# Optimization experiments

Measured on AMD Instinct MI355X. Metric: run time of the kernel, lower is better.

## Reference

```python
import jax, jax.numpy as jnp
import numpy as np

VOCAB = 32000
EMB = 1024
BLOCK = 2048
B = 4


def setup_inputs() -> dict:
    key = jax.random.key(0)
    ks = jax.random.split(key, 10)
    s = EMB ** -0.5
    return {
        "idx": jax.random.randint(ks[0], (B, BLOCK), 0, VOCAB),
        "targets": jax.random.randint(ks[1], (B, BLOCK), 0, VOCAB),
        "tok_emb": jax.random.normal(ks[2], (VOCAB, EMB), jnp.float32),
        "pos_emb": jax.random.normal(ks[3], (BLOCK, EMB), jnp.float32),
        "Wk": jax.random.normal(ks[4], (EMB, EMB), jnp.float32) * s,
        "Wq": jax.random.normal(ks[5], (EMB, EMB), jnp.float32) * s,
        "Wv": jax.random.normal(ks[6], (EMB, EMB), jnp.float32) * s,
        "Wlm": jax.random.normal(ks[7], (EMB, VOCAB), jnp.float32) * s,
        "blm": jnp.zeros((VOCAB,), jnp.float32),
    }


def reference(idx, targets, tok_emb, pos_emb, Wk, Wq, Wv, Wlm, blm):
    B_, T = idx.shape
    x = tok_emb[idx] + pos_emb[:T]  # [B,T,C]
    C = x.shape[-1]
    k = x @ Wk  # [B,T,H]
    q = x @ Wq
    v = x @ Wv
    wei = jnp.einsum("bth,bsh->bts", q, k) * (C ** -0.5)  # [B,T,T]
    causal = jnp.tril(jnp.ones((T, T), bool))
    wei = jnp.where(causal, wei, -jnp.inf)
    wei = jax.nn.softmax(wei, axis=-1)
    out = jnp.einsum("bts,bsh->bth", wei, v)  # [B,T,H]
    logits = out @ Wlm + blm  # [B,T,V]
    logits2d = logits.reshape(B_ * T, -1)
    tgt = targets.reshape(B_ * T)
    logp = jax.nn.log_softmax(logits2d, axis=-1)
    loss = -jnp.mean(jnp.take_along_axis(logp, tgt[:, None], axis=1))
    return logits2d, loss
```

## Files before the change

kernel.cpp:

```cpp
#include <hip/hip_runtime.h>
#include <hip/hip_bf16.h>
#include <cstdint>

#define VOCAB 32000
#define EMB   1024
#define TLEN  2048
#define NB    4
#define MTOT  (NB*TLEN)

typedef __bf16 bf16;
typedef __bf16 bf16x8 __attribute__((ext_vector_type(8)));
typedef float  f32x4  __attribute__((ext_vector_type(4)));

__global__ void embed_kernel(const int* __restrict__ idx,
                             const float* __restrict__ tok,
                             const float* __restrict__ pos,
                             bf16* __restrict__ x)
{
    int gid = blockIdx.x * 256 + threadIdx.x;
    int r   = gid >> 7;
    int c0  = (gid & 127) << 3;
    int t   = r & (TLEN - 1);
    int tk  = idx[r];
    const float4* tp = reinterpret_cast<const float4*>(tok + (long)tk * EMB + c0);
    const float4* pp = reinterpret_cast<const float4*>(pos + (long)t  * EMB + c0);
    float4 a0 = tp[0], a1 = tp[1];
    float4 b0 = pp[0], b1 = pp[1];
    bf16x8 o;
    o[0] = (bf16)(a0.x + b0.x); o[1] = (bf16)(a0.y + b0.y);
    o[2] = (bf16)(a0.z + b0.z); o[3] = (bf16)(a0.w + b0.w);
    o[4] = (bf16)(a1.x + b1.x); o[5] = (bf16)(a1.y + b1.y);
    o[6] = (bf16)(a1.z + b1.z); o[7] = (bf16)(a1.w + b1.w);
    *reinterpret_cast<bf16x8*>(x + (long)r * EMB + c0) = o;
}

__global__ void transpose_conv_kernel(const float* __restrict__ W,
                                      bf16* __restrict__ Wt,
                                      int Kdim, int Ndim)
{
    __shared__ bf16 tile[64][65];
    int n0 = blockIdx.x * 64;
    int k0 = blockIdx.y * 64;
    int tid = threadIdx.x;
    int c  = tid & 63, r0 = tid >> 6;
#pragma unroll
    for (int i = 0; i < 16; ++i) {
        int r = r0 + i * 4;
        tile[r][c] = (bf16)W[(long)(k0 + r) * Ndim + n0 + c];
    }
    __syncthreads();
    int kc = tid & 63, nr0 = tid >> 6;
#pragma unroll
    for (int i = 0; i < 16; ++i) {
        int nr = nr0 + i * 4;
        Wt[(long)(n0 + nr) * Kdim + k0 + kc] = tile[kc][nr];
    }
}

__device__ __forceinline__ void gll16(const void* g, void* l)
{
    __builtin_amdgcn_global_load_lds(
        (const __attribute__((address_space(1))) unsigned int*)g,
        (__attribute__((address_space(3))) unsigned int*)l, 16, 0, 0);
}

template<int OMODE>
__global__ __launch_bounds__(256)
void gemm_bt_kernel(const bf16* __restrict__ A, int lda, long sA,
                    const bf16* __restrict__ Bt, int ldb, long sB,
                    void* __restrict__ Cv, int ldc, long sC,
                    int K, const float* __restrict__ bias)
{
    __shared__ bf16 As[128 * 32];
    __shared__ bf16 Bs[128 * 32];

    const int tid  = threadIdx.x;
    const int lane = tid & 63;
    const int wv   = tid >> 6;
    const int wr   = wv >> 1, wc = wv & 1;
    const long zb  = blockIdx.z;

    const bf16* Ab = A  + zb * sA + (long)(blockIdx.y * 128) * lda;
    const bf16* Bb = Bt + zb * sB + (long)(blockIdx.x * 128) * ldb;

    f32x4 acc[4][4] = {};

    const int l0 = tid, l1 = tid + 256;
    const int r0s = l0 >> 2, kg0 = (l0 & 3) * 8;
    const int r1s = l1 >> 2, kg1 = (l1 & 3) * 8;

    for (int kt = 0; kt < K; kt += 32) {
        if (kt) __syncthreads();
        gll16(Ab + (long)r0s * lda + kt + kg0, &As[l0 * 8]);
        gll16(Ab + (long)r1s * lda + kt + kg1, &As[l1 * 8]);
        gll16(Bb + (long)r0s * ldb + kt + kg0, &Bs[l0 * 8]);
        gll16(Bb + (long)r1s * ldb + kt + kg1, &Bs[l1 * 8]);
        __syncthreads();

        bf16x8 af[4], bfr[4];
#pragma unroll
        for (int i = 0; i < 4; ++i) {
            af[i]  = *reinterpret_cast<const bf16x8*>(
                         &As[(wr * 64 + i * 16 + (lane & 15)) * 32 + (lane >> 4) * 8]);
            bfr[i] = *reinterpret_cast<const bf16x8*>(
                         &Bs[(wc * 64 + i * 16 + (lane & 15)) * 32 + (lane >> 4) * 8]);
        }
#pragma unroll
        for (int i = 0; i < 4; ++i)
#pragma unroll
            for (int j = 0; j < 4; ++j)
                acc[i][j] = __builtin_amdgcn_mfma_f32_16x16x32_bf16(
                                af[i], bfr[j], acc[i][j], 0, 0, 0);
    }

    const int rowb = blockIdx.y * 128 + wr * 64 + ((lane >> 4) << 2);
    const int colb = blockIdx.x * 128 + wc * 64 + (lane & 15);

    if (OMODE == 0) {
        bf16* C = (bf16*)Cv + zb * sC;
#pragma unroll
        for (int i = 0; i < 4; ++i)
#pragma unroll
            for (int j = 0; j < 4; ++j)
#pragma unroll
                for (int r = 0; r < 4; ++r)
                    C[(long)(rowb + i * 16 + r) * ldc + colb + j * 16] = (bf16)acc[i][j][r];
    } else {
        float* C = (float*)Cv + zb * sC;
#pragma unroll
        for (int i = 0; i < 4; ++i)
#pragma unroll
            for (int j = 0; j < 4; ++j)
#pragma unroll
                for (int r = 0; r < 4; ++r)
                    C[(long)(rowb + i * 16 + r) * ldc + colb + j * 16] = acc[i][j][r];
    }
}

__device__ __forceinline__ void stage256(const bf16* __restrict__ gbase, int kt,
                                         bf16* lbase, int tid)
{
#pragma unroll
    for (int p = 0; p < 4; ++p) {
        int lin  = p * 512 + tid;
        int row  = lin >> 3;
        int slot = lin & 7;
        int ke   = ((slot ^ (row & 7)) << 3) + kt;
        gll16(gbase + (long)row * EMB + ke, lbase + lin * 8);
    }
}

__global__ __launch_bounds__(512)
void gemm256_logits(const bf16* __restrict__ A, const bf16* __restrict__ Bt,
                    float* __restrict__ C, const float* __restrict__ bias,
                    float2* __restrict__ part)
{
    extern __shared__ bf16 smem[];
    bf16* As = smem;
    bf16* Bs = smem + 32768;

    const int tid  = threadIdx.x;
    const int lane = tid & 63, wid = tid >> 6;
    const int wr = wid >> 2, wc = wid & 3;
    const int l15 = lane & 15, hi = lane >> 4, l7 = lane & 7;

    const int wg = blockIdx.x;
    const int xcd = wg & 7, c = wg >> 3;
    const int nb = c >> 2;
    const int mb = xcd * 4 + (c & 3);

    const bf16* Ab = A  + (long)(mb * 256) * EMB;
    const bf16* Bb = Bt + (long)(nb * 256) * EMB;

    f32x4 acc[8][4] = {};

    stage256(Ab, 0, As, tid);
    stage256(Bb, 0, Bs, tid);
    __syncthreads();

    const int NT = EMB / 64;
    for (int t = 0; t < NT; ++t) {
        const int buf = t & 1;
        if (t + 1 < NT) {
            stage256(Ab, (t + 1) * 64, As + (buf ^ 1) * 16384, tid);
            stage256(Bb, (t + 1) * 64, Bs + (buf ^ 1) * 16384, tid);
        }
        const bf16* Ap = As + buf * 16384 + (wr * 128) * 64;
        const bf16* Bp = Bs + buf * 16384 + (wc * 64) * 64;
#pragma unroll
        for (int ks = 0; ks < 2; ++ks) {
            const int ko = 8 * (((ks << 2) | hi) ^ l7);
            bf16x8 bfr[4];
#pragma unroll
            for (int n = 0; n < 4; ++n)
                bfr[n] = *(const bf16x8*)(Bp + (n * 16 + l15) * 64 + ko);
#pragma unroll
            for (int m = 0; m < 8; ++m) {
                bf16x8 af = *(const bf16x8*)(Ap + (m * 16 + l15) * 64 + ko);
#pragma unroll
                for (int n = 0; n < 4; ++n)
                    acc[m][n] = __builtin_amdgcn_mfma_f32_16x16x32_bf16(
                                    af, bfr[n], acc[m][n], 0, 0, 0);
            }
        }
        __syncthreads();
    }

    float* pm = (float*)smem;
    float* ps = pm + 1024;

    const long colbase = (long)nb * 256 + wc * 64 + l15;
    float bv[4];
#pragma unroll
    for (int n = 0; n < 4; ++n) bv[n] = bias[colbase + n * 16];

    const long rowbase = (long)mb * 256 + wr * 128;
#pragma unroll
    for (int m = 0; m < 8; ++m) {
#pragma unroll
        for (int r = 0; r < 4; ++r) {
            float v0 = acc[m][0][r] + bv[0];
            float v1 = acc[m][1][r] + bv[1];
            float v2 = acc[m][2][r] + bv[2];
            float v3 = acc[m][3][r] + bv[3];
            long row = rowbase + m * 16 + (hi << 2) + r;
            float* Cp = C + row * (long)VOCAB + colbase;
            Cp[0] = v0; Cp[16] = v1; Cp[32] = v2; Cp[48] = v3;

            float lm = fmaxf(fmaxf(v0, v1), fmaxf(v2, v3));
#pragma unroll
            for (int o = 1; o < 16; o <<= 1) lm = fmaxf(lm, __shfl_xor(lm, o));
            float sp = __expf(v0 - lm) + __expf(v1 - lm) +
                       __expf(v2 - lm) + __expf(v3 - lm);
#pragma unroll
            for (int o = 1; o < 16; o <<= 1) sp += __shfl_xor(sp, o);
            if (l15 == 0) {
                int rb = wr * 128 + m * 16 + (hi << 2) + r;
                pm[wc * 256 + rb] = lm;
                ps[wc * 256 + rb] = sp;
            }
        }
    }
    __syncthreads();
    if (tid < 256) {
        float m0 = pm[tid], m1 = pm[256 + tid], m2 = pm[512 + tid], m3 = pm[768 + tid];
        float M = fmaxf(fmaxf(m0, m1), fmaxf(m2, m3));
        float S = ps[tid] * __expf(m0 - M) + ps[256 + tid] * __expf(m1 - M) +
                  ps[512 + tid] * __expf(m2 - M) + ps[768 + tid] * __expf(m3 - M);
        part[((long)mb * 256 + tid) * 125 + nb] = make_float2(M, S);
    }
}

__global__ void softmax_causal_kernel(const bf16* __restrict__ S,
                                      bf16* __restrict__ P)
{
    const int r = blockIdx.x;
    const int t = r & (TLEN - 1);
    const int tid = threadIdx.x;
    const int lane = tid & 63, wv = tid >> 6;
    const float scale = 0.03125f;
    const int c0 = tid * 8;
    bf16x8 sv = *(const bf16x8*)(S + (long)r * TLEN + c0);

    float v[8];
    float m = -1e30f;
#pragma unroll
    for (int i = 0; i < 8; ++i) {
        float x = (c0 + i <= t) ? (float)sv[i] * scale : -1e30f;
        v[i] = x;
        m = fmaxf(m, x);
    }
    __shared__ float red[4];
#pragma unroll
    for (int off = 32; off; off >>= 1) m = fmaxf(m, __shfl_xor(m, off));
    if (lane == 0) red[wv] = m;
    __syncthreads();
    m = fmaxf(fmaxf(red[0], red[1]), fmaxf(red[2], red[3]));
    __syncthreads();

    float s = 0.f;
#pragma unroll
    for (int i = 0; i < 8; ++i) { v[i] = __expf(v[i] - m); s += v[i]; }
#pragma unroll
    for (int off = 32; off; off >>= 1) s += __shfl_xor(s, off);
    if (lane == 0) red[wv] = s;
    __syncthreads();
    s = red[0] + red[1] + red[2] + red[3];
    float inv = 1.0f / s;
    bf16x8 o;
#pragma unroll
    for (int i = 0; i < 8; ++i) o[i] = (bf16)(v[i] * inv);
    *(bf16x8*)(P + (long)r * TLEN + c0) = o;
}

__global__ void loss_combine_kernel(const float2* __restrict__ part,
                                    const float* __restrict__ logits,
                                    const int* __restrict__ tgt,
                                    float* __restrict__ bsum)
{
    const int tid = threadIdx.x;
    const int row = blockIdx.x * 256 + tid;
    const int lane = tid & 63, wv = tid >> 6;
    const float2* p = part + (long)row * 125;
    float M = -1e30f, S = 0.f;
    for (int i = 0; i < 125; ++i) {
        float2 v = p[i];
        if (v.x <= M) S += v.y * __expf(v.x - M);
        else { S = S * __expf(M - v.x) + v.y; M = v.x; }
    }
    float lse = M + __logf(S);
    float l = lse - logits[(long)row * VOCAB + tgt[row]];
#pragma unroll
    for (int off = 32; off; off >>= 1) l += __shfl_xor(l, off);
    __shared__ float red[4];
    if (lane == 0) red[wv] = l;
    __syncthreads();
    if (tid == 0) bsum[blockIdx.x] = red[0] + red[1] + red[2] + red[3];
}

__global__ void loss_final_kernel(const float* __restrict__ bsum,
                                  float* __restrict__ out)
{
    const int lane = threadIdx.x;
    float s = (lane < 32) ? bsum[lane] : 0.f;
#pragma unroll
    for (int off = 32; off; off >>= 1) s += __shfl_xor(s, off);
    if (lane == 0) out[0] = s * (1.0f / MTOT);
}

extern "C" void kernel_launch(void* const* d_in, const int* in_sizes, int n_in,
                              void* d_out, int out_size, void* d_ws, size_t ws_size,
                              hipStream_t stream)
{
    const int*   idx = (const int*)  d_in[0];
    const int*   tgt = (const int*)  d_in[1];
    const float* tok = (const float*)d_in[2];
    const float* pos = (const float*)d_in[3];
    const float* Wk  = (const float*)d_in[4];
    const float* Wq  = (const float*)d_in[5];
    const float* Wv  = (const float*)d_in[6];
    const float* Wlm = (const float*)d_in[7];
    const float* blm = (const float*)d_in[8];
    float* out = (float*)d_out;

    char* ws = (char*)d_ws;
    if (ws_size < (size_t)140 * 1024 * 1024) return;

    bf16*   x     = (bf16*)(ws);
    bf16*   qk    = (bf16*)(ws + (16l << 20));
    bf16*   v_t   = (bf16*)(ws + (48l << 20));
    bf16*   S     = (bf16*)(ws + (64l << 20));
    bf16*   Wqk_t = (bf16*)(ws + (96l << 20));
    bf16*   Wv_t  = (bf16*)(ws + (100l << 20));
    bf16*   att   = (bf16*)(ws);
    bf16*   P     = (bf16*)(ws + (16l << 20));
    bf16*   Wlm_t = (bf16*)(ws + (48l << 20));
    float2* part  = (float2*)(ws + (112l << 20));
    float*  bsum  = (float*)(ws + (120l << 20));

    embed_kernel<<<dim3(MTOT * EMB / 8 / 256), 256, 0, stream>>>(idx, tok, pos, x);

    transpose_conv_kernel<<<dim3(16, 16), 256, 0, stream>>>(Wq, Wqk_t, EMB, EMB);
    transpose_conv_kernel<<<dim3(16, 16), 256, 0, stream>>>(Wk, Wqk_t + 1024 * 1024, EMB, EMB);
    transpose_conv_kernel<<<dim3(16, 16), 256, 0, stream>>>(Wv, Wv_t, EMB, EMB);

    gemm_bt_kernel<0><<<dim3(2048 / 128, MTOT / 128, 1), 256, 0, stream>>>(
        x, EMB, 0, Wqk_t, EMB, 0, qk, 2048, 0, EMB, nullptr);
    gemm_bt_kernel<0><<<dim3(MTOT / 128, EMB / 128, 1), 256, 0, stream>>>(
        Wv_t, EMB, 0, x, EMB, 0, v_t, MTOT, 0, EMB, nullptr);

    gemm_bt_kernel<0><<<dim3(TLEN / 128, TLEN / 128, NB), 256, 0, stream>>>(
        qk, 2048, (long)TLEN * 2048, qk + 1024, 2048, (long)TLEN * 2048,
        S, TLEN, (long)TLEN * TLEN, EMB, nullptr);

    softmax_causal_kernel<<<dim3(MTOT), 256, 0, stream>>>(S, P);

    gemm_bt_kernel<0><<<dim3(EMB / 128, TLEN / 128, NB), 256, 0, stream>>>(
        P, TLEN, (long)TLEN * TLEN, v_t, MTOT, (long)TLEN,
        att, EMB, (long)TLEN * EMB, TLEN, nullptr);

    transpose_conv_kernel<<<dim3(VOCAB / 64, EMB / 64), 256, 0, stream>>>(
        Wlm, Wlm_t, EMB, VOCAB);

    gemm256_logits<<<dim3(4000), 512, 131072, stream>>>(att, Wlm_t, out, blm, part);

    loss_combine_kernel<<<dim3(32), 256, 0, stream>>>(part, out, tgt, bsum);
    loss_final_kernel<<<dim3(1), 64, 0, stream>>>(bsum, out + (long)MTOT * VOCAB);
}
```

Before: 959.8 us.

## Restructure logits GEMM mainloop into 4-phase ping-pong with split-K staging

```diff
diff --git a/kernel.cpp b/kernel.cpp
--- a/kernel.cpp
+++ b/kernel.cpp
@@ -137,16 +137,14 @@
     }
 }
 
-__device__ __forceinline__ void stage256(const bf16* __restrict__ gbase, int kt,
-                                         bf16* lbase, int tid)
-{
-#pragma unroll
-    for (int p = 0; p < 4; ++p) {
-        int lin  = p * 512 + tid;
-        int row  = lin >> 3;
-        int slot = lin & 7;
-        int ke   = ((slot ^ (row & 7)) << 3) + kt;
-        gll16(gbase + (long)row * EMB + ke, lbase + lin * 8);
+__device__ __forceinline__ void stage_kh(const bf16* __restrict__ g, int koff,
+                                         bf16* l, int tid)
+{
+#pragma unroll
+    for (int p = 0; p < 2; ++p) {
+        int lin = p * 512 + tid;
+        int row = lin >> 2, gr = lin & 3;
+        gll16(g + (long)row * EMB + koff + gr * 8, l + lin * 8);
     }
 }
 
@@ -162,7 +160,7 @@
     const int tid  = threadIdx.x;
     const int lane = tid & 63, wid = tid >> 6;
     const int wr = wid >> 2, wc = wid & 3;
-    const int l15 = lane & 15, hi = lane >> 4, l7 = lane & 7;
+    const int l15 = lane & 15, hi = lane >> 4;
 
     const int wg = blockIdx.x;
     const int xcd = wg & 7, c = wg >> 3;
@@ -173,38 +171,79 @@
     const bf16* Bb = Bt + (long)(nb * 256) * EMB;
 
     f32x4 acc[8][4] = {};
-
-    stage256(Ab, 0, As, tid);
-    stage256(Bb, 0, Bs, tid);
-    __syncthreads();
-
-    const int NT = EMB / 64;
-    for (int t = 0; t < NT; ++t) {
-        const int buf = t & 1;
-        if (t + 1 < NT) {
-            stage256(Ab, (t + 1) * 64, As + (buf ^ 1) * 16384, tid);
-            stage256(Bb, (t + 1) * 64, Bs + (buf ^ 1) * 16384, tid);
-        }
-        const bf16* Ap = As + buf * 16384 + (wr * 128) * 64;
-        const bf16* Bp = Bs + buf * 16384 + (wc * 64) * 64;
-#pragma unroll
-        for (int ks = 0; ks < 2; ++ks) {
-            const int ko = 8 * (((ks << 2) | hi) ^ l7);
-            bf16x8 bfr[4];
-#pragma unroll
-            for (int n = 0; n < 4; ++n)
-                bfr[n] = *(const bf16x8*)(Bp + (n * 16 + l15) * 64 + ko);
-#pragma unroll
-            for (int m = 0; m < 8; ++m) {
-                bf16x8 af = *(const bf16x8*)(Ap + (m * 16 + l15) * 64 + ko);
-#pragma unroll
-                for (int n = 0; n < 4; ++n)
-                    acc[m][n] = __builtin_amdgcn_mfma_f32_16x16x32_bf16(
-                                    af, bfr[n], acc[m][n], 0, 0, 0);
-            }
-        }
-        __syncthreads();
-    }
+    bf16x8 af[4], bfr[4];
+
+    const int aoff = (wr * 128 + l15) * 32 + hi * 8;
+    const int boff = (wc * 64  + l15) * 32 + hi * 8;
+
+#define DSA(b,kh,m)  (*(const bf16x8*)(As + (b)*16384 + (kh)*8192 + (m)*512 + aoff))
+#define DSB(b,kh,n)  (*(const bf16x8*)(Bs + (b)*16384 + (kh)*8192 + (n)*512 + boff))
+
+#define MFMA_Q(mbase)                                                        \
+    __builtin_amdgcn_s_setprio(1);                                           \
+    _Pragma("unroll")                                                        \
+    for (int m_ = 0; m_ < 4; ++m_)                                           \
+        _Pragma("unroll")                                                    \
+        for (int n_ = 0; n_ < 4; ++n_)                                       \
+            acc[(mbase) + m_][n_] = __builtin_amdgcn_mfma_f32_16x16x32_bf16( \
+                af[m_], bfr[n_], acc[(mbase) + m_][n_], 0, 0, 0);            \
+    __builtin_amdgcn_s_setprio(0);
+
+#define PHASE_BAR                                                            \
+    __builtin_amdgcn_s_barrier();                                            \
+    asm volatile("s_waitcnt lgkmcnt(0)" ::: "memory");                       \
+    __builtin_amdgcn_sched_barrier(0);
+
+#define TILE(b, kt, DOSTAGE, LAST)                                           \
+    {                                                                        \
+                                                          \
+        _Pragma("unroll") for (int n_=0;n_<4;++n_) bfr[n_] = DSB(b,0,n_);    \
+        _Pragma("unroll") for (int m_=0;m_<4;++m_) af[m_]  = DSA(b,0,m_);    \
+        if (DOSTAGE) stage_kh(Ab, (kt)+64, As + ((b)^1)*16384, tid);         \
+        PHASE_BAR; MFMA_Q(0);                                                \
+        __builtin_amdgcn_s_barrier();                                        \
+                                              \
+        if (LAST) { asm volatile("s_waitcnt vmcnt(0)" ::: "memory"); }       \
+        else      { asm volatile("s_waitcnt vmcnt(2)" ::: "memory"); }       \
+        _Pragma("unroll") for (int m_=0;m_<4;++m_) af[m_]  = DSA(b,0,4+m_);  \
+        if (DOSTAGE) stage_kh(Bb, (kt)+64, Bs + ((b)^1)*16384, tid);         \
+        PHASE_BAR; MFMA_Q(4);                                                \
+        __builtin_amdgcn_s_barrier();                                        \
+                                                          \
+        _Pragma("unroll") for (int n_=0;n_<4;++n_) bfr[n_] = DSB(b,1,n_);    \
+        _Pragma("unroll") for (int m_=0;m_<4;++m_) af[m_]  = DSA(b,1,m_);    \
+        if (DOSTAGE) stage_kh(Ab, (kt)+96, As + ((b)^1)*16384 + 8192, tid);  \
+        PHASE_BAR; MFMA_Q(0);                                                \
+        __builtin_amdgcn_s_barrier();                                        \
+                                                          \
+        if (!LAST) { asm volatile("s_waitcnt vmcnt(2)" ::: "memory"); }      \
+        _Pragma("unroll") for (int m_=0;m_<4;++m_) af[m_]  = DSA(b,1,4+m_);  \
+        if (DOSTAGE) stage_kh(Bb, (kt)+96, Bs + ((b)^1)*16384 + 8192, tid);  \
+        PHASE_BAR; MFMA_Q(4);                                                \
+        __builtin_amdgcn_s_barrier();                                        \
+    }
+
+    stage_kh(Ab, 0,  As, tid);
+    stage_kh(Bb, 0,  Bs, tid);
+    stage_kh(Ab, 32, As + 8192, tid);
+    stage_kh(Bb, 32, Bs + 8192, tid);
+    asm volatile("s_waitcnt vmcnt(4)" ::: "memory");
+    __builtin_amdgcn_s_barrier();
+
+#pragma unroll 1
+    for (int it = 0; it < 7; ++it) {
+        const int kt = it * 128;
+        TILE(0, kt, 1, 0);
+        TILE(1, kt + 64, 1, 0);
+    }
+    TILE(0, 896, 1, 0);
+    TILE(1, 960, 0, 1);
+
+#undef TILE
+#undef PHASE_BAR
+#undef MFMA_Q
+#undef DSA
+#undef DSB
 
     float* pm = (float*)smem;
     float* ps = pm + 1024;
```

New measurement: 1.012 ms. 1.05x slower.

## Swizzle small-GEMM LDS layout and triple-buffer B in logits GEMM

Applied to the files above, without the earlier changes.

```diff
diff --git a/kernel.cpp b/kernel.cpp
--- a/kernel.cpp
+++ b/kernel.cpp
@@ -78,6 +78,7 @@
     const int lane = tid & 63;
     const int wv   = tid >> 6;
     const int wr   = wv >> 1, wc = wv & 1;
+    const int l15  = lane & 15, hi = lane >> 4;
     const long zb  = blockIdx.z;
 
     const bf16* Ab = A  + zb * sA + (long)(blockIdx.y * 128) * lda;
@@ -86,8 +87,10 @@
     f32x4 acc[4][4] = {};
 
     const int l0 = tid, l1 = tid + 256;
-    const int r0s = l0 >> 2, kg0 = (l0 & 3) * 8;
-    const int r1s = l1 >> 2, kg1 = (l1 & 3) * 8;
+    const int r0s = l0 >> 2, kg0 = (((l0 & 3) ^ (r0s & 3))) * 8;
+    const int r1s = l1 >> 2, kg1 = (((l1 & 3) ^ (r1s & 3))) * 8;
+    const int kofr = ( 0);
+    (void)kofr;
 
     for (int kt = 0; kt < K; kt += 32) {
         if (kt) __syncthreads();
@@ -97,13 +100,14 @@
         gll16(Bb + (long)r1s * ldb + kt + kg1, &Bs[l1 * 8]);
         __syncthreads();
 
+        const int kos = (hi ^ (l15 & 3)) * 8;
         bf16x8 af[4], bfr[4];
 #pragma unroll
         for (int i = 0; i < 4; ++i) {
             af[i]  = *reinterpret_cast<const bf16x8*>(
-                         &As[(wr * 64 + i * 16 + (lane & 15)) * 32 + (lane >> 4) * 8]);
+                         &As[(wr * 64 + i * 16 + l15) * 32 + kos]);
             bfr[i] = *reinterpret_cast<const bf16x8*>(
-                         &Bs[(wc * 64 + i * 16 + (lane & 15)) * 32 + (lane >> 4) * 8]);
+                         &Bs[(wc * 64 + i * 16 + l15) * 32 + kos]);
         }
 #pragma unroll
         for (int i = 0; i < 4; ++i)
@@ -113,8 +117,8 @@
                                 af[i], bfr[j], acc[i][j], 0, 0, 0);
     }
 
-    const int rowb = blockIdx.y * 128 + wr * 64 + ((lane >> 4) << 2);
-    const int colb = blockIdx.x * 128 + wc * 64 + (lane & 15);
+    const int rowb = blockIdx.y * 128 + wr * 64 + (hi << 2);
+    const int colb = blockIdx.x * 128 + wc * 64 + l15;
 
     if (OMODE == 0) {
         bf16* C = (bf16*)Cv + zb * sC;
@@ -174,36 +178,54 @@
 
     f32x4 acc[8][4] = {};
 
-    stage256(Ab, 0, As, tid);
-    stage256(Bb, 0, Bs, tid);
-    __syncthreads();
-
-    const int NT = EMB / 64;
-    for (int t = 0; t < NT; ++t) {
-        const int buf = t & 1;
-        if (t + 1 < NT) {
-            stage256(Ab, (t + 1) * 64, As + (buf ^ 1) * 16384, tid);
-            stage256(Bb, (t + 1) * 64, Bs + (buf ^ 1) * 16384, tid);
+    const int ko0 = 8 * (hi ^ l7);
+    const int ko1 = 8 * ((4 | hi) ^ l7);
+    const bf16* ApR = As + (wr * 128 + l15) * 64;
+    const bf16* BpR = Bs + (wc * 64  + l15) * 64;
+
+    stage256(Ab, 0,  As, tid);
+    stage256(Bb, 0,  Bs, tid);
+    stage256(Bb, 64, Bs + 16384, tid);
+    asm volatile("s_waitcnt vmcnt(4)" ::: "memory");
+    __builtin_amdgcn_sched_barrier(0);
+    __builtin_amdgcn_s_barrier();
+
+    int aB = 0, bB = 0;
+#pragma unroll 1
+    for (int t = 0; t < 16; ++t) {
+        if (t + 1 < 16)
+            stage256(Ab, (t + 1) * 64, As + (aB ^ 1) * 16384, tid);
+        if (t + 2 < 16) {
+            int b2 = bB + 2; if (b2 >= 3) b2 -= 3;
+            stage256(Bb, (t + 2) * 64, Bs + b2 * 16384, tid);
         }
-        const bf16* Ap = As + buf * 16384 + (wr * 128) * 64;
-        const bf16* Bp = Bs + buf * 16384 + (wc * 64) * 64;
+
+        const bf16* Ap = ApR + aB * 16384;
+        const bf16* Bp = BpR + bB * 16384;
 #pragma unroll
         for (int ks = 0; ks < 2; ++ks) {
-            const int ko = 8 * (((ks << 2) | hi) ^ l7);
+            const int ko = ks ? ko1 : ko0;
             bf16x8 bfr[4];
 #pragma unroll
             for (int n = 0; n < 4; ++n)
-                bfr[n] = *(const bf16x8*)(Bp + (n * 16 + l15) * 64 + ko);
+                bfr[n] = *(const bf16x8*)(Bp + n * 1024 + ko);
 #pragma unroll
             for (int m = 0; m < 8; ++m) {
-                bf16x8 af = *(const bf16x8*)(Ap + (m * 16 + l15) * 64 + ko);
+                bf16x8 af = *(const bf16x8*)(Ap + m * 1024 + ko);
 #pragma unroll
                 for (int n = 0; n < 4; ++n)
                     acc[m][n] = __builtin_amdgcn_mfma_f32_16x16x32_bf16(
                                     af, bfr[n], acc[m][n], 0, 0, 0);
             }
         }
-        __syncthreads();
+
+        if (t < 14)       { asm volatile("s_waitcnt vmcnt(4)" ::: "memory"); }
+        else if (t == 14) { asm volatile("s_waitcnt vmcnt(0)" ::: "memory"); }
+        __builtin_amdgcn_sched_barrier(0);
+        __builtin_amdgcn_s_barrier();
+
+        aB ^= 1;
+        bB = (bB == 2) ? 0 : bB + 1;
     }
 
     float* pm = (float*)smem;
@@ -382,7 +404,7 @@
     transpose_conv_kernel<<<dim3(VOCAB / 64, EMB / 64), 256, 0, stream>>>(
         Wlm, Wlm_t, EMB, VOCAB);
 
-    gemm256_logits<<<dim3(4000), 512, 131072, stream>>>(att, Wlm_t, out, blm, part);
+    gemm256_logits<<<dim3(4000), 512, 163840, stream>>>(att, Wlm_t, out, blm, part);
 
     loss_combine_kernel<<<dim3(32), 256, 0, stream>>>(part, out, tgt, bsum);
     loss_final_kernel<<<dim3(1), 64, 0, stream>>>(bsum, out + (long)MTOT * VOCAB);
```

Result: no change. 964.3 us (+0.5%).

## Skip masked causal tiles in attention GEMMs and swizzle LDS layout

Applied to the files above, without the earlier changes.

```diff
diff --git a/kernel.cpp b/kernel.cpp
--- a/kernel.cpp
+++ b/kernel.cpp
@@ -64,13 +64,15 @@
         (__attribute__((address_space(3))) unsigned int*)l, 16, 0, 0);
 }
 
-template<int OMODE>
+template<int OMODE, int CMODE>
 __global__ __launch_bounds__(256)
 void gemm_bt_kernel(const bf16* __restrict__ A, int lda, long sA,
                     const bf16* __restrict__ Bt, int ldb, long sB,
                     void* __restrict__ Cv, int ldc, long sC,
                     int K, const float* __restrict__ bias)
 {
+    if (CMODE == 1 && blockIdx.x > blockIdx.y) return;
+
     __shared__ bf16 As[128 * 32];
     __shared__ bf16 Bs[128 * 32];
 
@@ -78,18 +80,21 @@
     const int lane = tid & 63;
     const int wv   = tid >> 6;
     const int wr   = wv >> 1, wc = wv & 1;
+    const int l15  = lane & 15, hi = lane >> 4;
     const long zb  = blockIdx.z;
 
     const bf16* Ab = A  + zb * sA + (long)(blockIdx.y * 128) * lda;
     const bf16* Bb = Bt + zb * sB + (long)(blockIdx.x * 128) * ldb;
 
+    const int Keff = (CMODE == 2) ? (int)((blockIdx.y + 1) * 128) : K;
+
     f32x4 acc[4][4] = {};
 
     const int l0 = tid, l1 = tid + 256;
-    const int r0s = l0 >> 2, kg0 = (l0 & 3) * 8;
-    const int r1s = l1 >> 2, kg1 = (l1 & 3) * 8;
-
-    for (int kt = 0; kt < K; kt += 32) {
+    const int r0s = l0 >> 2, kg0 = ((l0 & 3) ^ ((r0s >> 1) & 3)) * 8;
+    const int r1s = l1 >> 2, kg1 = ((l1 & 3) ^ ((r1s >> 1) & 3)) * 8;
+
+    for (int kt = 0; kt < Keff; kt += 32) {
         if (kt) __syncthreads();
         gll16(Ab + (long)r0s * lda + kt + kg0, &As[l0 * 8]);
         gll16(Ab + (long)r1s * lda + kt + kg1, &As[l1 * 8]);
@@ -97,13 +102,14 @@
         gll16(Bb + (long)r1s * ldb + kt + kg1, &Bs[l1 * 8]);
         __syncthreads();
 
+        const int kos = (hi ^ ((l15 >> 1) & 3)) * 8;
         bf16x8 af[4], bfr[4];
 #pragma unroll
         for (int i = 0; i < 4; ++i) {
             af[i]  = *reinterpret_cast<const bf16x8*>(
-                         &As[(wr * 64 + i * 16 + (lane & 15)) * 32 + (lane >> 4) * 8]);
+                         &As[(wr * 64 + i * 16 + l15) * 32 + kos]);
             bfr[i] = *reinterpret_cast<const bf16x8*>(
-                         &Bs[(wc * 64 + i * 16 + (lane & 15)) * 32 + (lane >> 4) * 8]);
+                         &Bs[(wc * 64 + i * 16 + l15) * 32 + kos]);
         }
 #pragma unroll
         for (int i = 0; i < 4; ++i)
@@ -113,8 +119,8 @@
                                 af[i], bfr[j], acc[i][j], 0, 0, 0);
     }
 
-    const int rowb = blockIdx.y * 128 + wr * 64 + ((lane >> 4) << 2);
-    const int colb = blockIdx.x * 128 + wc * 64 + (lane & 15);
+    const int rowb = blockIdx.y * 128 + wr * 64 + (hi << 2);
+    const int colb = blockIdx.x * 128 + wc * 64 + l15;
 
     if (OMODE == 0) {
         bf16* C = (bf16*)Cv + zb * sC;
@@ -256,19 +262,25 @@
 {
     const int r = blockIdx.x;
     const int t = r & (TLEN - 1);
+    const int limit = ((t >> 7) + 1) << 7;
     const int tid = threadIdx.x;
     const int lane = tid & 63, wv = tid >> 6;
     const float scale = 0.03125f;
     const int c0 = tid * 8;
-    bf16x8 sv = *(const bf16x8*)(S + (long)r * TLEN + c0);
 
     float v[8];
     float m = -1e30f;
-#pragma unroll
-    for (int i = 0; i < 8; ++i) {
-        float x = (c0 + i <= t) ? (float)sv[i] * scale : -1e30f;
-        v[i] = x;
-        m = fmaxf(m, x);
+    if (c0 < limit) {
+        bf16x8 sv = *(const bf16x8*)(S + (long)r * TLEN + c0);
+#pragma unroll
+        for (int i = 0; i < 8; ++i) {
+            float x = (c0 + i <= t) ? (float)sv[i] * scale : -1e30f;
+            v[i] = x;
+            m = fmaxf(m, x);
+        }
+    } else {
+#pragma unroll
+        for (int i = 0; i < 8; ++i) v[i] = -1e30f;
     }
     __shared__ float red[4];
 #pragma unroll
@@ -287,10 +299,12 @@
     __syncthreads();
     s = red[0] + red[1] + red[2] + red[3];
     float inv = 1.0f / s;
-    bf16x8 o;
-#pragma unroll
-    for (int i = 0; i < 8; ++i) o[i] = (bf16)(v[i] * inv);
-    *(bf16x8*)(P + (long)r * TLEN + c0) = o;
+    if (c0 < limit) {
+        bf16x8 o;
+#pragma unroll
+        for (int i = 0; i < 8; ++i) o[i] = (bf16)(v[i] * inv);
+        *(bf16x8*)(P + (long)r * TLEN + c0) = o;
+    }
 }
 
 __global__ void loss_combine_kernel(const float2* __restrict__ part,
@@ -364,18 +378,18 @@
     transpose_conv_kernel<<<dim3(16, 16), 256, 0, stream>>>(Wk, Wqk_t + 1024 * 1024, EMB, EMB);
     transpose_conv_kernel<<<dim3(16, 16), 256, 0, stream>>>(Wv, Wv_t, EMB, EMB);
 
-    gemm_bt_kernel<0><<<dim3(2048 / 128, MTOT / 128, 1), 256, 0, stream>>>(
+    gemm_bt_kernel<0,0><<<dim3(2048 / 128, MTOT / 128, 1), 256, 0, stream>>>(
         x, EMB, 0, Wqk_t, EMB, 0, qk, 2048, 0, EMB, nullptr);
-    gemm_bt_kernel<0><<<dim3(MTOT / 128, EMB / 128, 1), 256, 0, stream>>>(
+    gemm_bt_kernel<0,0><<<dim3(MTOT / 128, EMB / 128, 1), 256, 0, stream>>>(
         Wv_t, EMB, 0, x, EMB, 0, v_t, MTOT, 0, EMB, nullptr);
 
-    gemm_bt_kernel<0><<<dim3(TLEN / 128, TLEN / 128, NB), 256, 0, stream>>>(
+    gemm_bt_kernel<0,1><<<dim3(TLEN / 128, TLEN / 128, NB), 256, 0, stream>>>(
         qk, 2048, (long)TLEN * 2048, qk + 1024, 2048, (long)TLEN * 2048,
         S, TLEN, (long)TLEN * TLEN, EMB, nullptr);
 
     softmax_causal_kernel<<<dim3(MTOT), 256, 0, stream>>>(S, P);
 
-    gemm_bt_kernel<0><<<dim3(EMB / 128, TLEN / 128, NB), 256, 0, stream>>>(
+    gemm_bt_kernel<0,2><<<dim3(EMB / 128, TLEN / 128, NB), 256, 0, stream>>>(
         P, TLEN, (long)TLEN * TLEN, v_t, MTOT, (long)TLEN,
         att, EMB, (long)TLEN * EMB, TLEN, nullptr);
 
```

New measurement: 952.0 us. No clear change (-0.8%).
